# Kernel optimization log

Hardware: AMD Instinct MI355X
Metric: run time of the kernel (lower is better)

## Reference

```python
import jax, jax.numpy as jnp
import numpy as np

V, D, B, NEG = 100000, 128, 4096, 5
D_INNER = int(D * 2.0 * 2 / 3)  # nGPT FF inner dim = 170

def l2norm(t, axis=-1):
    return t / jnp.linalg.norm(t, axis=axis, keepdims=True)

def setup_inputs() -> dict:
    key = jax.random.key(0)
    ks = jax.random.split(key, 8)
    return {
        "input_ids": jax.random.randint(ks[0], (B,), 0, V),
        "target_ids": jax.random.randint(ks[1], (B,), 0, V),
        "neg_ids": jax.random.randint(ks[2], (B, NEG), 0, V),
        "W_in": jax.random.normal(ks[3], (V, D), jnp.float32) * (1.0 / np.sqrt(D)),
        "W_out": jax.random.normal(ks[4], (V, D), jnp.float32) * (1.0 / np.sqrt(D)),
        "W_hidden": jax.random.normal(ks[5], (D_INNER, D), jnp.float32) * 0.02,
        "W_gate": jax.random.normal(ks[6], (D_INNER, D), jnp.float32) * 0.02,
        "W_ff_out": jax.random.normal(ks[7], (D, D_INNER), jnp.float32) * 0.02,
        "hidden_scale": jnp.ones((D_INNER,), jnp.float32),
        "gate_scale": jnp.ones((D_INNER,), jnp.float32),
        "logit_scale": jnp.full((V,), D ** -0.5, dtype=jnp.float32),  # Scale param init = s_logit_scale
    }

def reference(input_ids, target_ids, neg_ids, W_in, W_out, W_hidden, W_gate,
              W_ff_out, hidden_scale, gate_scale, logit_scale):
    # skipgram: gather normalized input embeddings
    emb = l2norm(W_in)[input_ids]                                  # (B, D)
    # nGPT FeedForward: silu-gated, weights l2-normalized on input dim
    h = (emb @ l2norm(W_hidden).T) * hidden_scale                  # (B, D_INNER)
    g = (emb @ l2norm(W_gate).T) * gate_scale * jnp.sqrt(jnp.float32(D))
    x = jax.nn.silu(g) * h
    x = x @ l2norm(W_ff_out, axis=0).T                             # (B, D), to_out norm_dim_in=False
    # logits over full vocab, scaled by Scale(): param * (init/scale)
    scale_eff = logit_scale * (1.0 / (D ** -0.5))                  # (V,)
    logits = (x @ l2norm(W_out).T) * scale_eff                     # (B, V)
    # negative-sampling loss: gather positive + sampled negative logits
    pos = jnp.take_along_axis(logits, target_ids[:, None], axis=1)  # (B, 1)
    neg = jnp.take_along_axis(logits, neg_ids, axis=1)              # (B, NEG)
    positive_loss = jax.nn.log_sigmoid(pos).mean()
    negative_loss = jax.nn.log_sigmoid(-neg).mean()
    return -(positive_loss + negative_loss)
```

## Files before the change

### kernel.cpp

```cpp
#include <hip/hip_runtime.h>
#include <math.h>

#define DD   128
#define DI   170
#define BB   4096
#define NNEG 5
#define ROWS 16
#define NBLK (BB / ROWS)
#define SQRT_D 11.3137084989847603904f

__device__ __forceinline__ float wave_bcast_sum(float v) {
#pragma unroll
    for (int m = 1; m < 64; m <<= 1) v += __shfl_xor(v, m, 64);
    return v;
}

__global__ __launch_bounds__(256) void norms_kernel(
    const float* __restrict__ W_hidden,
    const float* __restrict__ W_gate,
    const float* __restrict__ W_ff_out,
    float* __restrict__ inv_h,
    float* __restrict__ inv_g,
    float* __restrict__ inv_f,
    float* __restrict__ out)
{
    if (blockIdx.x == 0 && threadIdx.x == 0) out[0] = 0.0f;
    const int wave = threadIdx.x >> 6;
    const int lane = threadIdx.x & 63;
    const int v = blockIdx.x * 4 + wave;
    if (v >= 3 * DI) return;
    float s;
    if (v < 2 * DI) {
        const float* W = (v < DI) ? W_hidden : W_gate;
        const int row = (v < DI) ? v : v - DI;
        float2 p = ((const float2*)(W + (long)row * DD))[lane];
        s = p.x * p.x + p.y * p.y;
    } else {
        const int c = v - 2 * DI;
        float a = W_ff_out[(long)(2 * lane)     * DI + c];
        float b = W_ff_out[(long)(2 * lane + 1) * DI + c];
        s = a * a + b * b;
    }
    s = wave_bcast_sum(s);
    if (lane == 0) {
        float inv = rsqrtf(s);
        if (v < DI)            inv_h[v] = inv;
        else if (v < 2 * DI)   inv_g[v - DI] = inv;
        else                   inv_f[v - 2 * DI] = inv;
    }
}

__global__ __launch_bounds__(256) void main_kernel(
    const int*   __restrict__ input_ids,
    const int*   __restrict__ target_ids,
    const int*   __restrict__ neg_ids,
    const float* __restrict__ W_in,
    const float* __restrict__ W_out,
    const float* __restrict__ W_hidden,
    const float* __restrict__ W_gate,
    const float* __restrict__ W_ff_out,
    const float* __restrict__ hidden_scale,
    const float* __restrict__ gate_scale,
    const float* __restrict__ logit_scale,
    const float* __restrict__ inv_h,
    const float* __restrict__ inv_g,
    const float* __restrict__ inv_f,
    float* __restrict__ out)
{
    __shared__ float s_emb[ROWS][DD];
    __shared__ float s_x[ROWS][DI + 2];
    __shared__ float s_xout[ROWS][DD];
    __shared__ float s_red[4];

    const int tid  = threadIdx.x;
    const int wave = tid >> 6;
    const int lane = tid & 63;
    const int b0   = blockIdx.x * ROWS;

#pragma unroll
    for (int k = 0; k < ROWS / 4; ++k) {
        const int r  = wave + 4 * k;
        const int id = input_ids[b0 + r];
        float2 p = ((const float2*)(W_in + (long)id * DD))[lane];
        float s  = wave_bcast_sum(p.x * p.x + p.y * p.y);
        float inv = rsqrtf(s);
        s_emb[r][2 * lane]     = p.x * inv;
        s_emb[r][2 * lane + 1] = p.y * inv;
    }
    __syncthreads();

    if (tid < DI) {
        const int i = tid;
        float ah[ROWS], ag[ROWS];
#pragma unroll
        for (int r = 0; r < ROWS; ++r) { ah[r] = 0.0f; ag[r] = 0.0f; }
        const float4* wh = (const float4*)(W_hidden + (long)i * DD);
        const float4* wg = (const float4*)(W_gate   + (long)i * DD);
        for (int d4 = 0; d4 < DD / 4; ++d4) {
            float4 h4 = wh[d4];
            float4 g4 = wg[d4];
#pragma unroll
            for (int r = 0; r < ROWS; ++r) {
                float4 e4 = ((const float4*)s_emb[r])[d4];
                ah[r] += e4.x * h4.x + e4.y * h4.y + e4.z * h4.z + e4.w * h4.w;
                ag[r] += e4.x * g4.x + e4.y * g4.y + e4.z * g4.z + e4.w * g4.w;
            }
        }
        const float hs = hidden_scale[i] * inv_h[i];
        const float gs = gate_scale[i]   * inv_g[i] * SQRT_D;
        const float fi = inv_f[i];
#pragma unroll
        for (int r = 0; r < ROWS; ++r) {
            float h = ah[r] * hs;
            float g = ag[r] * gs;
            float x = (g / (1.0f + __expf(-g))) * h;
            s_x[r][i] = x * fi;
        }
    }
    __syncthreads();

    {
        const int dd = tid & 127;
        const int r0 = tid >> 7;
        float acc[ROWS / 2];
#pragma unroll
        for (int k = 0; k < ROWS / 2; ++k) acc[k] = 0.0f;
        const float2* wrow = (const float2*)(W_ff_out + (long)dd * DI);
        for (int i2 = 0; i2 < DI / 2; ++i2) {
            float2 wf = wrow[i2];
#pragma unroll
            for (int k = 0; k < ROWS / 2; ++k) {
                const int r = r0 + 2 * k;
                float2 xv = *(const float2*)&s_x[r][2 * i2];
                acc[k] += xv.x * wf.x + xv.y * wf.y;
            }
        }
#pragma unroll
        for (int k = 0; k < ROWS / 2; ++k) s_xout[r0 + 2 * k][dd] = acc[k];
    }
    __syncthreads();

    float wacc = 0.0f;
    for (int t = wave; t < ROWS * (1 + NNEG); t += 4) {
        const int r  = t / (1 + NNEG);
        const int jj = t % (1 + NNEG);
        const int bidx = b0 + r;
        const int id = (jj == 0) ? target_ids[bidx] : neg_ids[bidx * NNEG + jj - 1];
        const float* wrow = W_out + (long)id * DD;
        float w0 = wrow[lane], w1 = wrow[64 + lane];
        float x0 = s_xout[r][lane], x1 = s_xout[r][64 + lane];
        float dot = w0 * x0 + w1 * x1;
        float ss  = w0 * w0 + w1 * w1;
#pragma unroll
        for (int m = 1; m < 64; m <<= 1) {
            dot += __shfl_xor(dot, m, 64);
            ss  += __shfl_xor(ss,  m, 64);
        }
        const float logit = dot * rsqrtf(ss) * logit_scale[id] * SQRT_D;
        const float z  = (jj == 0) ? logit : -logit;
        const float ls = fminf(z, 0.0f) - log1pf(__expf(-fabsf(z)));
        wacc += (jj == 0) ? ls * (1.0f / BB) : ls * (1.0f / (BB * NNEG));
    }
    if (lane == 0) s_red[wave] = wacc;
    __syncthreads();
    if (tid == 0) {
        float tot = s_red[0] + s_red[1] + s_red[2] + s_red[3];
        atomicAdd(out, -tot);
    }
}

extern "C" void kernel_launch(void* const* d_in, const int* in_sizes, int n_in,
                              void* d_out, int out_size, void* d_ws, size_t ws_size,
                              hipStream_t stream) {
    (void)in_sizes; (void)n_in; (void)out_size; (void)ws_size;
    const int*   input_ids    = (const int*)  d_in[0];
    const int*   target_ids   = (const int*)  d_in[1];
    const int*   neg_ids      = (const int*)  d_in[2];
    const float* W_in         = (const float*)d_in[3];
    const float* W_out        = (const float*)d_in[4];
    const float* W_hidden     = (const float*)d_in[5];
    const float* W_gate       = (const float*)d_in[6];
    const float* W_ff_out     = (const float*)d_in[7];
    const float* hidden_scale = (const float*)d_in[8];
    const float* gate_scale   = (const float*)d_in[9];
    const float* logit_scale  = (const float*)d_in[10];
    float* out   = (float*)d_out;
    float* inv_h = (float*)d_ws;
    float* inv_g = inv_h + DI;
    float* inv_f = inv_g + DI;

    norms_kernel<<<128, 256, 0, stream>>>(W_hidden, W_gate, W_ff_out,
                                          inv_h, inv_g, inv_f, out);
    main_kernel<<<NBLK, 256, 0, stream>>>(input_ids, target_ids, neg_ids,
                                          W_in, W_out, W_hidden, W_gate, W_ff_out,
                                          hidden_scale, gate_scale, logit_scale,
                                          inv_h, inv_g, inv_f, out);
}
```

Measured before the change: 172.5 us.

## Halve rows per block, batch gather loads, unroll loops, restructure norms kernel

```diff
diff --git a/kernel.cpp b/kernel.cpp
--- a/kernel.cpp
+++ b/kernel.cpp
@@ -5,8 +5,10 @@
 #define DI   170
 #define BB   4096
 #define NNEG 5
-#define ROWS 16
+#define ROWS 8
 #define NBLK (BB / ROWS)
+#define TASKS (ROWS * (1 + NNEG))
+#define TPW  (TASKS / 4)
 #define SQRT_D 11.3137084989847603904f
 
 __device__ __forceinline__ float wave_bcast_sum(float v) {
@@ -25,28 +27,29 @@
     float* __restrict__ out)
 {
     if (blockIdx.x == 0 && threadIdx.x == 0) out[0] = 0.0f;
-    const int wave = threadIdx.x >> 6;
-    const int lane = threadIdx.x & 63;
-    const int v = blockIdx.x * 4 + wave;
-    if (v >= 3 * DI) return;
-    float s;
-    if (v < 2 * DI) {
+    if (blockIdx.x < 85) {
+        const int wave = threadIdx.x >> 6;
+        const int lane = threadIdx.x & 63;
+        const int v = blockIdx.x * 4 + wave;
         const float* W = (v < DI) ? W_hidden : W_gate;
         const int row = (v < DI) ? v : v - DI;
         float2 p = ((const float2*)(W + (long)row * DD))[lane];
-        s = p.x * p.x + p.y * p.y;
+        float s = wave_bcast_sum(p.x * p.x + p.y * p.y);
+        if (lane == 0) {
+            float inv = rsqrtf(s);
+            if (v < DI) inv_h[v] = inv; else inv_g[v - DI] = inv;
+        }
     } else {
-        const int c = v - 2 * DI;
-        float a = W_ff_out[(long)(2 * lane)     * DI + c];
-        float b = W_ff_out[(long)(2 * lane + 1) * DI + c];
-        s = a * a + b * b;
-    }
-    s = wave_bcast_sum(s);
-    if (lane == 0) {
-        float inv = rsqrtf(s);
-        if (v < DI)            inv_h[v] = inv;
-        else if (v < 2 * DI)   inv_g[v - DI] = inv;
-        else                   inv_f[v - 2 * DI] = inv;
+        const int c = threadIdx.x;
+        if (c < DI) {
+            float s = 0.0f;
+#pragma unroll 4
+            for (int d = 0; d < DD; ++d) {
+                float a = W_ff_out[(long)d * DI + c];
+                s += a * a;
+            }
+            inv_f[c] = rsqrtf(s);
+        }
     }
 }
 
@@ -96,6 +99,7 @@
         for (int r = 0; r < ROWS; ++r) { ah[r] = 0.0f; ag[r] = 0.0f; }
         const float4* wh = (const float4*)(W_hidden + (long)i * DD);
         const float4* wg = (const float4*)(W_gate   + (long)i * DD);
+#pragma unroll 4
         for (int d4 = 0; d4 < DD / 4; ++d4) {
             float4 h4 = wh[d4];
             float4 g4 = wg[d4];
@@ -126,6 +130,7 @@
 #pragma unroll
         for (int k = 0; k < ROWS / 2; ++k) acc[k] = 0.0f;
         const float2* wrow = (const float2*)(W_ff_out + (long)dd * DI);
+#pragma unroll 5
         for (int i2 = 0; i2 < DI / 2; ++i2) {
             float2 wf = wrow[i2];
 #pragma unroll
@@ -140,8 +145,11 @@
     }
     __syncthreads();
 
-    float wacc = 0.0f;
-    for (int t = wave; t < ROWS * (1 + NNEG); t += 4) {
+    float dotp[TPW], ssp[TPW], lsc[TPW];
+    const int tbase = wave * TPW;
+#pragma unroll
+    for (int k = 0; k < TPW; ++k) {
+        const int t  = tbase + k;
         const int r  = t / (1 + NNEG);
         const int jj = t % (1 + NNEG);
         const int bidx = b0 + r;
@@ -149,14 +157,21 @@
         const float* wrow = W_out + (long)id * DD;
         float w0 = wrow[lane], w1 = wrow[64 + lane];
         float x0 = s_xout[r][lane], x1 = s_xout[r][64 + lane];
-        float dot = w0 * x0 + w1 * x1;
-        float ss  = w0 * w0 + w1 * w1;
+        dotp[k] = w0 * x0 + w1 * x1;
+        ssp[k]  = w0 * w0 + w1 * w1;
+        lsc[k]  = logit_scale[id];
+    }
+    float wacc = 0.0f;
+#pragma unroll
+    for (int k = 0; k < TPW; ++k) {
+        float dot = dotp[k], ss = ssp[k];
 #pragma unroll
         for (int m = 1; m < 64; m <<= 1) {
             dot += __shfl_xor(dot, m, 64);
             ss  += __shfl_xor(ss,  m, 64);
         }
-        const float logit = dot * rsqrtf(ss) * logit_scale[id] * SQRT_D;
+        const int jj = (tbase + k) % (1 + NNEG);
+        const float logit = dot * rsqrtf(ss) * lsc[k] * SQRT_D;
         const float z  = (jj == 0) ? logit : -logit;
         const float ls = fminf(z, 0.0f) - log1pf(__expf(-fabsf(z)));
         wacc += (jj == 0) ? ls * (1.0f / BB) : ls * (1.0f / (BB * NNEG));
@@ -189,8 +204,8 @@
     float* inv_g = inv_h + DI;
     float* inv_f = inv_g + DI;
 
-    norms_kernel<<<128, 256, 0, stream>>>(W_hidden, W_gate, W_ff_out,
-                                          inv_h, inv_g, inv_f, out);
+    norms_kernel<<<86, 256, 0, stream>>>(W_hidden, W_gate, W_ff_out,
+                                         inv_h, inv_g, inv_f, out);
     main_kernel<<<NBLK, 256, 0, stream>>>(input_ids, target_ids, neg_ids,
                                           W_in, W_out, W_hidden, W_gate, W_ff_out,
                                           hidden_scale, gate_scale, logit_scale,
```

New measurement: 174.0 us. About the same (+0.9%).
